# Kernel optimization log

Hardware: AMD Instinct MI355X
Metric: run time of the kernel (lower is better)

## Reference

```python
import jax, jax.numpy as jnp
import numpy as np

EMBED = 256
HEADS = 8
N_EDGES = 32  # topk k per query node = head_edges * heads = number_of_edges
HEAD_DIM = EMBED // HEADS


def setup_inputs() -> dict:
    key = jax.random.key(0)
    k1, k2, k3, k4 = jax.random.split(key, 4)
    B, L = 8, 2048
    return {
        "keys": jax.random.normal(k1, (B, L, EMBED), dtype=jnp.float32),
        "query": jax.random.normal(k2, (B, L, EMBED), dtype=jnp.float32),
        "Wk": jax.random.normal(k3, (HEAD_DIM, HEAD_DIM), dtype=jnp.float32) / np.sqrt(HEAD_DIM).astype(np.float32),
        "Wq": jax.random.normal(k4, (HEAD_DIM, HEAD_DIM), dtype=jnp.float32) / np.sqrt(HEAD_DIM).astype(np.float32),
    }


def reference(keys, query, Wk, Wq):
    B, Lk, _ = keys.shape
    Lq = query.shape[1]
    # split heads: [B, L, H, D]
    k = keys.reshape(B, Lk, HEADS, HEAD_DIM)
    q = query.reshape(B, Lq, HEADS, HEAD_DIM)
    # per-head linear projections (torch Linear: y = x @ W^T, no bias)
    k = jnp.einsum('nkhd,ed->nkhe', k, Wk)
    q = jnp.einsum('nqhd,ed->nqhe', q, Wq)
    # attention scores [B, H, Lq, Lk]
    energy = jnp.einsum('nqhd,nkhd->nhqk', q, k)
    attn = jax.nn.softmax(energy / jnp.sqrt(jnp.float32(EMBED)), axis=3)
    # mean over heads -> [B, Lq, Lk]
    mean_attn = jnp.mean(attn, axis=1)
    # topk neighbor indices per query node, then sorted ascending
    _, idx = jax.lax.top_k(mean_attn, N_EDGES)          # [B, Lq, N_EDGES]
    edges = jnp.sort(idx, axis=2)
    nodes = jnp.broadcast_to(jnp.arange(Lq, dtype=edges.dtype)[None, :, None], edges.shape)
    # edge_index [B, 2, Lq * N_EDGES]: row0 = source node, row1 = neighbor
    edge_index = jnp.stack([nodes.reshape(B, -1), edges.reshape(B, -1)], axis=1)
    return edge_index
```

## Files before the change

### kernel.cpp

```cpp
#include <hip/hip_runtime.h>
#include <hip/hip_bf16.h>

#define NB 8
#define LSEQ 2048
#define HH 8
#define DD 32
#define EE 256
#define NE 32
#define QT 16
#define NTH 1024
#define KW 128
#define NTILE 8
#define SMS 2050

#define ZQT 64
#define ZNT 512
#define ZKW 256
#define ZNTILE 16

typedef __attribute__((ext_vector_type(8))) short short8;
typedef __attribute__((ext_vector_type(4))) float f32x4;

__global__ __launch_bounds__(256) void proj_kernel(const float* __restrict__ x,
                                                   const float* __restrict__ W,
                                                   float scale,
                                                   __hip_bfloat16* __restrict__ o1,
                                                   __hip_bfloat16* __restrict__ o2,
                                                   __hip_bfloat16* __restrict__ o3) {
  const int b = blockIdx.x;
  __shared__ float xs[EE];
  __shared__ float Ws[DD][DD + 1];
  const int t = threadIdx.x;
  xs[t] = x[(size_t)b * EE + t];
  for (int i = t; i < DD * DD; i += 256) Ws[i / DD][i % DD] = W[i];
  __syncthreads();
  const int h = t / DD, e = t % DD;
  float acc = 0.f;
#pragma unroll
  for (int d = 0; d < DD; ++d) acc = fmaf(xs[h * DD + d], Ws[e][d], acc);
  acc *= scale;
  const int n = b / LSEQ, l = b % LSEQ;
  const size_t oi = (((size_t)n * HH + h) * LSEQ + l) * DD + e;
  __hip_bfloat16 p1 = __float2bfloat16(acc);
  float r1 = acc - __bfloat162float(p1);
  __hip_bfloat16 p2 = __float2bfloat16(r1);
  float r2 = r1 - __bfloat162float(p2);
  __hip_bfloat16 p3 = __float2bfloat16(r2);
  o1[oi] = p1;
  o2[oi] = p2;
  o3[oi] = p3;
}

__global__ __launch_bounds__(ZNT) void zinv_kernel(
    const __hip_bfloat16* __restrict__ q1, const __hip_bfloat16* __restrict__ q2,
    const __hip_bfloat16* __restrict__ q3, const __hip_bfloat16* __restrict__ k1,
    const __hip_bfloat16* __restrict__ k2, const __hip_bfloat16* __restrict__ k3,
    float* __restrict__ invp) {
  __shared__ float zlds[HH][ZQT];

  const int t = threadIdx.x;
  const int w = t >> 6, l = t & 63;
  const int g = l >> 4, c = l & 15;
  const int n = blockIdx.x & 7;
  const int q0 = (blockIdx.x >> 3) * ZQT;

  ((float*)zlds)[t] = 0.f;
  __syncthreads();

  for (int h = 0; h < HH; ++h) {
    const size_t hb = ((size_t)n * HH + h) * LSEQ;
    short8 aH[4], aM[4], aL[4];
#pragma unroll
    for (int qs = 0; qs < 4; ++qs) {
      const size_t qoff = (hb + q0 + qs * 16 + c) * DD + (size_t)g * 8;
      aH[qs] = *(const short8*)(q1 + qoff);
      aM[qs] = *(const short8*)(q2 + qoff);
      aL[qs] = *(const short8*)(q3 + qoff);
    }
    float Zl[4][4];
#pragma unroll
    for (int qs = 0; qs < 4; ++qs)
#pragma unroll
      for (int r = 0; r < 4; ++r) Zl[qs][r] = 0.f;

    for (int t2 = 0; t2 < ZNTILE; ++t2) {
      const size_t koff = (hb + (size_t)w * ZKW + t2 * 16 + c) * DD + (size_t)g * 8;
      const short8 bH = *(const short8*)(k1 + koff);
      const short8 bM = *(const short8*)(k2 + koff);
      const short8 bL = *(const short8*)(k3 + koff);
#pragma unroll
      for (int qs = 0; qs < 4; ++qs) {
        f32x4 a = {0.f, 0.f, 0.f, 0.f};
        a = __builtin_amdgcn_mfma_f32_16x16x32_bf16(aH[qs], bH, a, 0, 0, 0);
        a = __builtin_amdgcn_mfma_f32_16x16x32_bf16(aH[qs], bM, a, 0, 0, 0);
        a = __builtin_amdgcn_mfma_f32_16x16x32_bf16(aM[qs], bH, a, 0, 0, 0);
        a = __builtin_amdgcn_mfma_f32_16x16x32_bf16(aH[qs], bL, a, 0, 0, 0);
        a = __builtin_amdgcn_mfma_f32_16x16x32_bf16(aL[qs], bH, a, 0, 0, 0);
        a = __builtin_amdgcn_mfma_f32_16x16x32_bf16(aM[qs], bM, a, 0, 0, 0);
#pragma unroll
        for (int r = 0; r < 4; ++r) Zl[qs][r] += exp2f(a[r]);
      }
    }
#pragma unroll
    for (int msk = 1; msk <= 8; msk <<= 1)
#pragma unroll
      for (int qs = 0; qs < 4; ++qs)
#pragma unroll
        for (int r = 0; r < 4; ++r) Zl[qs][r] += __shfl_xor(Zl[qs][r], msk);
    if (c == 0) {
#pragma unroll
      for (int qs = 0; qs < 4; ++qs)
#pragma unroll
        for (int r = 0; r < 4; ++r) atomicAdd(&zlds[h][qs * 16 + g * 4 + r], Zl[qs][r]);
    }
  }
  __syncthreads();
  const int h2 = t >> 6, qi = t & 63;
  invp[((size_t)n * HH + h2) * LSEQ + q0 + qi] = __builtin_amdgcn_rcpf(zlds[h2][qi]);
}

__global__ __launch_bounds__(NTH) void attn_topk_kernel(
    const __hip_bfloat16* __restrict__ q1, const __hip_bfloat16* __restrict__ q2,
    const __hip_bfloat16* __restrict__ q3, const __hip_bfloat16* __restrict__ k1,
    const __hip_bfloat16* __restrict__ k2, const __hip_bfloat16* __restrict__ k3,
    const float* __restrict__ invp, int* __restrict__ out) {
  __shared__ float smean[QT * SMS];
  __shared__ float ilds[HH][QT];

  const int t = threadIdx.x;
  const int w = t >> 6, l = t & 63;
  const int g = l >> 4, c = l & 15;
  const int n = blockIdx.x & 7;
  const int q0 = (blockIdx.x >> 3) * QT;

  for (int i = t; i < QT * SMS; i += NTH) smean[i] = 0.f;
  if (t < HH * QT) {
    const int h = t >> 4, qi = t & 15;
    ilds[h][qi] = invp[((size_t)n * HH + h) * LSEQ + q0 + qi];
  }
  float* macc = &smean[(g * 4) * SMS + w * KW + c];
  __syncthreads();

  for (int h = 0; h < HH; ++h) {
    const size_t hb = ((size_t)n * HH + h) * LSEQ;
    const size_t qoff = (hb + q0 + c) * DD + (size_t)g * 8;
    const short8 aH = *(const short8*)(q1 + qoff);
    const short8 aM = *(const short8*)(q2 + qoff);
    const short8 aL = *(const short8*)(q3 + qoff);
    float iv[4];
#pragma unroll
    for (int r = 0; r < 4; ++r) iv[r] = ilds[h][g * 4 + r];

#pragma unroll
    for (int t2 = 0; t2 < NTILE; ++t2) {
      const size_t koff = (hb + (size_t)w * KW + t2 * 16 + c) * DD + (size_t)g * 8;
      const short8 bH = *(const short8*)(k1 + koff);
      const short8 bM = *(const short8*)(k2 + koff);
      const short8 bL = *(const short8*)(k3 + koff);
      f32x4 a = {0.f, 0.f, 0.f, 0.f};
      a = __builtin_amdgcn_mfma_f32_16x16x32_bf16(aH, bH, a, 0, 0, 0);
      a = __builtin_amdgcn_mfma_f32_16x16x32_bf16(aH, bM, a, 0, 0, 0);
      a = __builtin_amdgcn_mfma_f32_16x16x32_bf16(aM, bH, a, 0, 0, 0);
      a = __builtin_amdgcn_mfma_f32_16x16x32_bf16(aH, bL, a, 0, 0, 0);
      a = __builtin_amdgcn_mfma_f32_16x16x32_bf16(aL, bH, a, 0, 0, 0);
      a = __builtin_amdgcn_mfma_f32_16x16x32_bf16(aM, bM, a, 0, 0, 0);
#pragma unroll
      for (int r = 0; r < 4; ++r) {
        float* p = macc + r * SMS + t2 * 16;
        *p = fmaf(exp2f(a[r]), iv[r], *p);
      }
    }
  }
  __syncthreads();

  float* row = &smean[w * SMS];
  float vals[32];
  float v1 = -1e30f, v2 = -1e30f;
  int i1 = 1 << 30, i2 = 1 << 30;
#pragma unroll
  for (int j = 0; j < 32; ++j) {
    float v = row[j * 64 + l];
    vals[j] = v;
    const int k = j * 64 + l;
    if (v > v1) { v2 = v1; i2 = i1; v1 = v; i1 = k; }
    else if (v > v2) { v2 = v; i2 = k; }
  }
  unsigned rem = 0u;
  int selk = 0;
#pragma unroll 1
  for (int it = 0; it < NE; ++it) {
    float bv = v1;
    int bk = i1;
#pragma unroll
    for (int off = 32; off >= 1; off >>= 1) {
      float ov = __shfl_xor(bv, off);
      int ok = __shfl_xor(bk, off);
      if (ov > bv || (ov == bv && ok < bk)) { bv = ov; bk = ok; }
    }
    if (l == it) selk = bk;
    if (i1 == bk) {
      rem |= 1u << (bk >> 6);
      if (i2 != (1 << 30)) {
        v1 = v2; i1 = i2;
        v2 = -1e30f; i2 = 1 << 30;
      } else {
        v1 = -1e30f; i1 = 1 << 30;
        v2 = -1e30f; i2 = 1 << 30;
#pragma unroll
        for (int j = 0; j < 32; ++j) {
          float v = ((rem >> j) & 1u) ? -1e30f : vals[j];
          const int k = j * 64 + l;
          if (v > v1) { v2 = v1; i2 = i1; v1 = v; i1 = k; }
          else if (v > v2) { v2 = v; i2 = k; }
        }
      }
    }
  }

  int rank = 0;
#pragma unroll
  for (int j = 0; j < NE; ++j) {
    int o = __shfl(selk, j);
    rank += (o < selk) ? 1 : 0;
  }
  const int qg = q0 + w;
  if (l < NE) {
    int* o0 = out + (size_t)n * 2 * LSEQ * NE + (size_t)qg * NE;
    int* o1p = o0 + (size_t)LSEQ * NE;
    o0[l] = qg;
    o1p[rank] = selk;
  }
}

extern "C" void kernel_launch(void* const* d_in, const int* in_sizes, int n_in,
                              void* d_out, int out_size, void* d_ws, size_t ws_size,
                              hipStream_t stream) {
  const float* keys = (const float*)d_in[0];
  const float* query = (const float*)d_in[1];
  const float* Wk = (const float*)d_in[2];
  const float* Wq = (const float*)d_in[3];
  int* out = (int*)d_out;

  const size_t SPLIT = (size_t)NB * HH * LSEQ * DD;
  __hip_bfloat16* qs1 = (__hip_bfloat16*)d_ws;
  __hip_bfloat16* qs2 = qs1 + SPLIT;
  __hip_bfloat16* qs3 = qs2 + SPLIT;
  __hip_bfloat16* ks1 = qs3 + SPLIT;
  __hip_bfloat16* ks2 = ks1 + SPLIT;
  __hip_bfloat16* ks3 = ks2 + SPLIT;
  float* invp = (float*)(ks3 + SPLIT);

  proj_kernel<<<NB * LSEQ, 256, 0, stream>>>(query, Wq, 0.0625f * 1.44269504088896340736f,
                                             qs1, qs2, qs3);
  proj_kernel<<<NB * LSEQ, 256, 0, stream>>>(keys, Wk, 1.0f, ks1, ks2, ks3);
  zinv_kernel<<<NB * (LSEQ / ZQT), ZNT, 0, stream>>>(qs1, qs2, qs3, ks1, ks2, ks3, invp);
  attn_topk_kernel<<<NB * (LSEQ / QT), NTH, 0, stream>>>(qs1, qs2, qs3, ks1, ks2, ks3, invp, out);
}
```

Before: 526.0 us.

## Split key dimension into quarters with per-chunk top-k and a merge kernel

The fused attention+topk kernel now processes 64 query rows against a 512-key chunk per block. Each block does a partial top-32 per row and writes candidate values and indices to workspace. A new merge kernel then picks the final top-32 from the 128 candidates and sorts the indices. The aim is more query reuse per block, a smaller per-row selection scan and more parallelism, paid for with an extra launch, a candidate round-trip through global memory and added syncthreads inside the head loop.

```diff
diff --git a/kernel.cpp b/kernel.cpp
--- a/kernel.cpp
+++ b/kernel.cpp
@@ -7,16 +7,16 @@
 #define DD 32
 #define EE 256
 #define NE 32
-#define QT 16
-#define NTH 1024
-#define KW 128
-#define NTILE 8
-#define SMS 2050
 
 #define ZQT 64
 #define ZNT 512
 #define ZKW 256
 #define ZNTILE 16
+
+#define MQT 64
+#define MKQ 512
+#define MNT 512
+#define MSMS 514
 
 typedef __attribute__((ext_vector_type(8))) short short8;
 typedef __attribute__((ext_vector_type(4))) float f32x4;
@@ -119,102 +119,153 @@
   invp[((size_t)n * HH + h2) * LSEQ + q0 + qi] = __builtin_amdgcn_rcpf(zlds[h2][qi]);
 }
 
-__global__ __launch_bounds__(NTH) void attn_topk_kernel(
+__global__ __launch_bounds__(MNT) void mean_topk_kernel(
     const __hip_bfloat16* __restrict__ q1, const __hip_bfloat16* __restrict__ q2,
     const __hip_bfloat16* __restrict__ q3, const __hip_bfloat16* __restrict__ k1,
     const __hip_bfloat16* __restrict__ k2, const __hip_bfloat16* __restrict__ k3,
-    const float* __restrict__ invp, int* __restrict__ out) {
-  __shared__ float smean[QT * SMS];
-  __shared__ float ilds[HH][QT];
+    const float* __restrict__ invp, float* __restrict__ candV,
+    int* __restrict__ candI) {
+  __shared__ float smean[MQT * MSMS];
+  __shared__ float ilds[HH][MQT];
 
   const int t = threadIdx.x;
   const int w = t >> 6, l = t & 63;
   const int g = l >> 4, c = l & 15;
+  const int qs = w >> 1, ks = w & 1;
   const int n = blockIdx.x & 7;
-  const int q0 = (blockIdx.x >> 3) * QT;
-
-  for (int i = t; i < QT * SMS; i += NTH) smean[i] = 0.f;
-  if (t < HH * QT) {
-    const int h = t >> 4, qi = t & 15;
+  const int rest = blockIdx.x >> 3;
+  const int qt = rest & 31;
+  const int kq = rest >> 5;
+  const int q0 = qt * MQT;
+  const int k0 = kq * MKQ;
+
+  for (int i = t; i < MQT * MSMS; i += MNT) smean[i] = 0.f;
+  for (int i = t; i < HH * MQT; i += MNT) {
+    const int h = i >> 6, qi = i & 63;
     ilds[h][qi] = invp[((size_t)n * HH + h) * LSEQ + q0 + qi];
   }
-  float* macc = &smean[(g * 4) * SMS + w * KW + c];
+  float* macc = &smean[(qs * 16 + g * 4) * MSMS + ks * 256 + c];
   __syncthreads();
 
   for (int h = 0; h < HH; ++h) {
     const size_t hb = ((size_t)n * HH + h) * LSEQ;
-    const size_t qoff = (hb + q0 + c) * DD + (size_t)g * 8;
+    const size_t qoff = (hb + q0 + qs * 16 + c) * DD + (size_t)g * 8;
     const short8 aH = *(const short8*)(q1 + qoff);
     const short8 aM = *(const short8*)(q2 + qoff);
     const short8 aL = *(const short8*)(q3 + qoff);
     float iv[4];
 #pragma unroll
-    for (int r = 0; r < 4; ++r) iv[r] = ilds[h][g * 4 + r];
-
-#pragma unroll
-    for (int t2 = 0; t2 < NTILE; ++t2) {
-      const size_t koff = (hb + (size_t)w * KW + t2 * 16 + c) * DD + (size_t)g * 8;
-      const short8 bH = *(const short8*)(k1 + koff);
-      const short8 bM = *(const short8*)(k2 + koff);
-      const short8 bL = *(const short8*)(k3 + koff);
-      f32x4 a = {0.f, 0.f, 0.f, 0.f};
-      a = __builtin_amdgcn_mfma_f32_16x16x32_bf16(aH, bH, a, 0, 0, 0);
-      a = __builtin_amdgcn_mfma_f32_16x16x32_bf16(aH, bM, a, 0, 0, 0);
-      a = __builtin_amdgcn_mfma_f32_16x16x32_bf16(aM, bH, a, 0, 0, 0);
-      a = __builtin_amdgcn_mfma_f32_16x16x32_bf16(aH, bL, a, 0, 0, 0);
-      a = __builtin_amdgcn_mfma_f32_16x16x32_bf16(aL, bH, a, 0, 0, 0);
-      a = __builtin_amdgcn_mfma_f32_16x16x32_bf16(aM, bM, a, 0, 0, 0);
-#pragma unroll
-      for (int r = 0; r < 4; ++r) {
-        float* p = macc + r * SMS + t2 * 16;
-        *p = fmaf(exp2f(a[r]), iv[r], *p);
+    for (int r = 0; r < 4; ++r) iv[r] = ilds[h][qs * 16 + g * 4 + r];
+
+    for (int sub = 0; sub < 4; ++sub) {
+#pragma unroll
+      for (int t2i = 0; t2i < 4; ++t2i) {
+        const int t2 = sub * 4 + t2i;
+        const size_t koff =
+            (hb + k0 + ks * 256 + t2 * 16 + c) * DD + (size_t)g * 8;
+        const short8 bH = *(const short8*)(k1 + koff);
+        const short8 bM = *(const short8*)(k2 + koff);
+        const short8 bL = *(const short8*)(k3 + koff);
+        f32x4 a = {0.f, 0.f, 0.f, 0.f};
+        a = __builtin_amdgcn_mfma_f32_16x16x32_bf16(aH, bH, a, 0, 0, 0);
+        a = __builtin_amdgcn_mfma_f32_16x16x32_bf16(aH, bM, a, 0, 0, 0);
+        a = __builtin_amdgcn_mfma_f32_16x16x32_bf16(aM, bH, a, 0, 0, 0);
+        a = __builtin_amdgcn_mfma_f32_16x16x32_bf16(aH, bL, a, 0, 0, 0);
+        a = __builtin_amdgcn_mfma_f32_16x16x32_bf16(aL, bH, a, 0, 0, 0);
+        a = __builtin_amdgcn_mfma_f32_16x16x32_bf16(aM, bM, a, 0, 0, 0);
+#pragma unroll
+        for (int r = 0; r < 4; ++r) {
+          float* p = macc + r * MSMS + t2 * 16;
+          *p = fmaf(exp2f(a[r]), iv[r], *p);
+        }
       }
-    }
-  }
-  __syncthreads();
-
-  float* row = &smean[w * SMS];
-  float vals[32];
-  float v1 = -1e30f, v2 = -1e30f;
-  int i1 = 1 << 30, i2 = 1 << 30;
-#pragma unroll
-  for (int j = 0; j < 32; ++j) {
-    float v = row[j * 64 + l];
-    vals[j] = v;
-    const int k = j * 64 + l;
-    if (v > v1) { v2 = v1; i2 = i1; v1 = v; i1 = k; }
-    else if (v > v2) { v2 = v; i2 = k; }
-  }
-  unsigned rem = 0u;
+      __syncthreads();
+    }
+  }
+
+#pragma unroll 1
+  for (int rr = 0; rr < 8; ++rr) {
+    const int row = w * 8 + rr;
+    float* rowp = &smean[row * MSMS];
+    float vals[8];
+    float v1 = -1e30f, v2 = -1e30f;
+    int i1 = 1 << 30, i2 = 1 << 30;
+#pragma unroll
+    for (int j = 0; j < 8; ++j) {
+      float v = rowp[j * 64 + l];
+      vals[j] = v;
+      const int k = j * 64 + l;
+      if (v > v1) { v2 = v1; i2 = i1; v1 = v; i1 = k; }
+      else if (v > v2) { v2 = v; i2 = k; }
+    }
+    unsigned rem = 0u;
+    int selk = 0;
+    float selv = 0.f;
+#pragma unroll 1
+    for (int it = 0; it < NE; ++it) {
+      float bv = v1;
+      int bk = i1;
+#pragma unroll
+      for (int off = 32; off >= 1; off >>= 1) {
+        float ov = __shfl_xor(bv, off);
+        int ok = __shfl_xor(bk, off);
+        if (ov > bv || (ov == bv && ok < bk)) { bv = ov; bk = ok; }
+      }
+      if (l == it) { selk = bk; selv = bv; }
+      if (i1 == bk) {
+        rem |= 1u << (bk >> 6);
+        if (i2 != (1 << 30)) {
+          v1 = v2; i1 = i2;
+          v2 = -1e30f; i2 = 1 << 30;
+        } else {
+          v1 = -1e30f; i1 = 1 << 30;
+          v2 = -1e30f; i2 = 1 << 30;
+#pragma unroll
+          for (int j = 0; j < 8; ++j) {
+            float v = ((rem >> j) & 1u) ? -1e30f : vals[j];
+            const int k = j * 64 + l;
+            if (v > v1) { v2 = v1; i2 = i1; v1 = v; i1 = k; }
+            else if (v > v2) { v2 = v; i2 = k; }
+          }
+        }
+      }
+    }
+    if (l < NE) {
+      const size_t cb = (((size_t)n * LSEQ + q0 + row) * 4 + kq) * NE;
+      candV[cb + l] = selv;
+      candI[cb + l] = k0 + selk;
+    }
+  }
+}
+
+__global__ __launch_bounds__(512) void merge_kernel(const float* __restrict__ candV,
+                                                    const int* __restrict__ candI,
+                                                    int* __restrict__ out) {
+  const int t = threadIdx.x;
+  const int w = t >> 6, l = t & 63;
+  const size_t rowg = (size_t)blockIdx.x * 8 + w;
+  const int n = (int)(rowg >> 11), q = (int)(rowg & 2047);
+  const size_t cb = rowg * 128;
+
+  float v0 = candV[cb + l], v1 = candV[cb + 64 + l];
+  int i0 = candI[cb + l], i1 = candI[cb + 64 + l];
+
   int selk = 0;
 #pragma unroll 1
   for (int it = 0; it < NE; ++it) {
-    float bv = v1;
-    int bk = i1;
+    float bv;
+    int bi;
+    if (v0 > v1 || (v0 == v1 && i0 < i1)) { bv = v0; bi = i0; }
+    else { bv = v1; bi = i1; }
 #pragma unroll
     for (int off = 32; off >= 1; off >>= 1) {
       float ov = __shfl_xor(bv, off);
-      int ok = __shfl_xor(bk, off);
-      if (ov > bv || (ov == bv && ok < bk)) { bv = ov; bk = ok; }
-    }
-    if (l == it) selk = bk;
-    if (i1 == bk) {
-      rem |= 1u << (bk >> 6);
-      if (i2 != (1 << 30)) {
-        v1 = v2; i1 = i2;
-        v2 = -1e30f; i2 = 1 << 30;
-      } else {
-        v1 = -1e30f; i1 = 1 << 30;
-        v2 = -1e30f; i2 = 1 << 30;
-#pragma unroll
-        for (int j = 0; j < 32; ++j) {
-          float v = ((rem >> j) & 1u) ? -1e30f : vals[j];
-          const int k = j * 64 + l;
-          if (v > v1) { v2 = v1; i2 = i1; v1 = v; i1 = k; }
-          else if (v > v2) { v2 = v; i2 = k; }
-        }
-      }
-    }
+      int oi = __shfl_xor(bi, off);
+      if (ov > bv || (ov == bv && oi < bi)) { bv = ov; bi = oi; }
+    }
+    if (l == it) selk = bi;
+    if (i0 == bi) v0 = -1e30f;
+    if (i1 == bi) v1 = -1e30f;
   }
 
   int rank = 0;
@@ -223,11 +274,10 @@
     int o = __shfl(selk, j);
     rank += (o < selk) ? 1 : 0;
   }
-  const int qg = q0 + w;
   if (l < NE) {
-    int* o0 = out + (size_t)n * 2 * LSEQ * NE + (size_t)qg * NE;
+    int* o0 = out + (size_t)n * 2 * LSEQ * NE + (size_t)q * NE;
     int* o1p = o0 + (size_t)LSEQ * NE;
-    o0[l] = qg;
+    o0[l] = q;
     o1p[rank] = selk;
   }
 }
@@ -249,10 +299,14 @@
   __hip_bfloat16* ks2 = ks1 + SPLIT;
   __hip_bfloat16* ks3 = ks2 + SPLIT;
   float* invp = (float*)(ks3 + SPLIT);
+  float* candV = invp + (size_t)NB * HH * LSEQ;
+  int* candI = (int*)(candV + (size_t)NB * LSEQ * 4 * NE);
 
   proj_kernel<<<NB * LSEQ, 256, 0, stream>>>(query, Wq, 0.0625f * 1.44269504088896340736f,
                                              qs1, qs2, qs3);
   proj_kernel<<<NB * LSEQ, 256, 0, stream>>>(keys, Wk, 1.0f, ks1, ks2, ks3);
   zinv_kernel<<<NB * (LSEQ / ZQT), ZNT, 0, stream>>>(qs1, qs2, qs3, ks1, ks2, ks3, invp);
-  attn_topk_kernel<<<NB * (LSEQ / QT), NTH, 0, stream>>>(qs1, qs2, qs3, ks1, ks2, ks3, invp, out);
-}
+  mean_topk_kernel<<<NB * (LSEQ / MQT) * 4, MNT, 0, stream>>>(qs1, qs2, qs3, ks1, ks2, ks3,
+                                                              invp, candV, candI);
+  merge_kernel<<<NB * LSEQ / 8, 512, 0, stream>>>(candV, candI, out);
+}
```

Measured after the change: 1.262 ms. 2.4x slower.

## Split key dimension in half with per-half top-k and a merge kernel

Applied to the files above, without the earlier changes.

The attention/top-k kernel now processes half of the keys per block, doubling the grid and halving shared memory per block (1024-wide mean rows). Each half writes its local top-32 values and indices to a workspace, and a new merge kernel picks the global top-32 from the 64 candidates and sorts them. This aims to raise occupancy and parallelism, since the old kernel used about 131KB of LDS per block. The cost is an extra launch, extra global traffic for candidates, and a serial merge loop.

```diff
diff --git a/kernel.cpp b/kernel.cpp
--- a/kernel.cpp
+++ b/kernel.cpp
@@ -9,9 +9,10 @@
 #define NE 32
 #define QT 16
 #define NTH 1024
-#define KW 128
-#define NTILE 8
-#define SMS 2050
+#define KHALF 1024
+#define KW 64
+#define NTILE 4
+#define SMS 1026
 
 #define ZQT 64
 #define ZNT 512
@@ -119,11 +120,12 @@
   invp[((size_t)n * HH + h2) * LSEQ + q0 + qi] = __builtin_amdgcn_rcpf(zlds[h2][qi]);
 }
 
-__global__ __launch_bounds__(NTH) void attn_topk_kernel(
+__global__ __launch_bounds__(NTH) void mean_topk_kernel(
     const __hip_bfloat16* __restrict__ q1, const __hip_bfloat16* __restrict__ q2,
     const __hip_bfloat16* __restrict__ q3, const __hip_bfloat16* __restrict__ k1,
     const __hip_bfloat16* __restrict__ k2, const __hip_bfloat16* __restrict__ k3,
-    const float* __restrict__ invp, int* __restrict__ out) {
+    const float* __restrict__ invp, float* __restrict__ candV,
+    int* __restrict__ candI) {
   __shared__ float smean[QT * SMS];
   __shared__ float ilds[HH][QT];
 
@@ -131,7 +133,11 @@
   const int w = t >> 6, l = t & 63;
   const int g = l >> 4, c = l & 15;
   const int n = blockIdx.x & 7;
-  const int q0 = (blockIdx.x >> 3) * QT;
+  const int rest = blockIdx.x >> 3;
+  const int qt = rest & 127;
+  const int half = rest >> 7;
+  const int q0 = qt * QT;
+  const int k0 = half * KHALF;
 
   for (int i = t; i < QT * SMS; i += NTH) smean[i] = 0.f;
   if (t < HH * QT) {
@@ -153,7 +159,7 @@
 
 #pragma unroll
     for (int t2 = 0; t2 < NTILE; ++t2) {
-      const size_t koff = (hb + (size_t)w * KW + t2 * 16 + c) * DD + (size_t)g * 8;
+      const size_t koff = (hb + k0 + (size_t)w * KW + t2 * 16 + c) * DD + (size_t)g * 8;
       const short8 bH = *(const short8*)(k1 + koff);
       const short8 bM = *(const short8*)(k2 + koff);
       const short8 bL = *(const short8*)(k3 + koff);
@@ -174,11 +180,11 @@
   __syncthreads();
 
   float* row = &smean[w * SMS];
-  float vals[32];
+  float vals[16];
   float v1 = -1e30f, v2 = -1e30f;
   int i1 = 1 << 30, i2 = 1 << 30;
 #pragma unroll
-  for (int j = 0; j < 32; ++j) {
+  for (int j = 0; j < 16; ++j) {
     float v = row[j * 64 + l];
     vals[j] = v;
     const int k = j * 64 + l;
@@ -187,6 +193,7 @@
   }
   unsigned rem = 0u;
   int selk = 0;
+  float selv = 0.f;
 #pragma unroll 1
   for (int it = 0; it < NE; ++it) {
     float bv = v1;
@@ -197,7 +204,7 @@
       int ok = __shfl_xor(bk, off);
       if (ov > bv || (ov == bv && ok < bk)) { bv = ov; bk = ok; }
     }
-    if (l == it) selk = bk;
+    if (l == it) { selk = bk; selv = bv; }
     if (i1 == bk) {
       rem |= 1u << (bk >> 6);
       if (i2 != (1 << 30)) {
@@ -207,7 +214,7 @@
         v1 = -1e30f; i1 = 1 << 30;
         v2 = -1e30f; i2 = 1 << 30;
 #pragma unroll
-        for (int j = 0; j < 32; ++j) {
+        for (int j = 0; j < 16; ++j) {
           float v = ((rem >> j) & 1u) ? -1e30f : vals[j];
           const int k = j * 64 + l;
           if (v > v1) { v2 = v1; i2 = i1; v1 = v; i1 = k; }
@@ -216,6 +223,38 @@
       }
     }
   }
+  if (l < NE) {
+    const size_t cb = (((size_t)n * LSEQ + q0 + w) * 2 + half) * NE;
+    candV[cb + l] = selv;
+    candI[cb + l] = k0 + selk;
+  }
+}
+
+__global__ __launch_bounds__(512) void merge_kernel(const float* __restrict__ candV,
+                                                    const int* __restrict__ candI,
+                                                    int* __restrict__ out) {
+  const int t = threadIdx.x;
+  const int w = t >> 6, l = t & 63;
+  const size_t rowg = (size_t)blockIdx.x * 8 + w;
+  const int n = (int)(rowg >> 11), q = (int)(rowg & 2047);
+
+  float v0 = candV[rowg * 64 + l];
+  int i0 = candI[rowg * 64 + l];
+
+  int selk = 0;
+#pragma unroll 1
+  for (int it = 0; it < NE; ++it) {
+    float bv = v0;
+    int bi = i0;
+#pragma unroll
+    for (int off = 32; off >= 1; off >>= 1) {
+      float ov = __shfl_xor(bv, off);
+      int oi = __shfl_xor(bi, off);
+      if (ov > bv || (ov == bv && oi < bi)) { bv = ov; bi = oi; }
+    }
+    if (l == it) selk = bi;
+    if (i0 == bi) v0 = -1e30f;
+  }
 
   int rank = 0;
 #pragma unroll
@@ -223,11 +262,10 @@
     int o = __shfl(selk, j);
     rank += (o < selk) ? 1 : 0;
   }
-  const int qg = q0 + w;
   if (l < NE) {
-    int* o0 = out + (size_t)n * 2 * LSEQ * NE + (size_t)qg * NE;
+    int* o0 = out + (size_t)n * 2 * LSEQ * NE + (size_t)q * NE;
     int* o1p = o0 + (size_t)LSEQ * NE;
-    o0[l] = qg;
+    o0[l] = q;
     o1p[rank] = selk;
   }
 }
@@ -249,10 +287,14 @@
   __hip_bfloat16* ks2 = ks1 + SPLIT;
   __hip_bfloat16* ks3 = ks2 + SPLIT;
   float* invp = (float*)(ks3 + SPLIT);
+  float* candV = invp + (size_t)NB * HH * LSEQ;
+  int* candI = (int*)(candV + (size_t)NB * LSEQ * 2 * NE);
 
   proj_kernel<<<NB * LSEQ, 256, 0, stream>>>(query, Wq, 0.0625f * 1.44269504088896340736f,
                                              qs1, qs2, qs3);
   proj_kernel<<<NB * LSEQ, 256, 0, stream>>>(keys, Wk, 1.0f, ks1, ks2, ks3);
   zinv_kernel<<<NB * (LSEQ / ZQT), ZNT, 0, stream>>>(qs1, qs2, qs3, ks1, ks2, ks3, invp);
-  attn_topk_kernel<<<NB * (LSEQ / QT), NTH, 0, stream>>>(qs1, qs2, qs3, ks1, ks2, ks3, invp, out);
-}
+  mean_topk_kernel<<<NB * (LSEQ / QT) * 2, NTH, 0, stream>>>(qs1, qs2, qs3, ks1, ks2, ks3,
+                                                             invp, candV, candI);
+  merge_kernel<<<NB * LSEQ / 8, 512, 0, stream>>>(candV, candI, out);
+}
```

After: 672.7 us. +27.9%, slower.
